# Kernel tuning notes

Hardware: AMD Instinct MI355X
Metric: run time of the kernel (lower is better)

Reference implementation:

```python
import jax, jax.numpy as jnp
import numpy as np

B, S, D = 4, 1024, 768
V, L, K = 50265, 256, 4
COMMIT = 0.25
PERP_W = 0.1


def _l2n(a):
    return a * jax.lax.rsqrt(jnp.sum(a * a, axis=-1, keepdims=True) + 1e-12)


def setup_inputs() -> dict:
    key = jax.random.key(0)
    ks = jax.random.split(key, 4)
    return {
        'x': jax.random.normal(ks[0], (B, S, D), dtype=jnp.float32),
        'codebook': jax.random.normal(ks[1], (V, D), dtype=jnp.float32) * 0.02,
        'W_in': jax.random.normal(ks[2], (D, L), dtype=jnp.float32) / np.sqrt(D),
        'b_in': jnp.zeros((L,), dtype=jnp.float32),
        'W_code': jax.random.normal(ks[3], (D, L), dtype=jnp.float32) / np.sqrt(D),
        'b_code': jnp.zeros((L,), dtype=jnp.float32),
    }


def reference(x, codebook, W_in, b_in, W_code, b_code):
    # project inputs and codebook to latent space, L2-normalize
    zi = _l2n(x.reshape(-1, D) @ W_in + b_in)                 # [N, L]
    # original normalizes latent codebook twice (idempotent) then stop-grads
    zc = jax.lax.stop_gradient(_l2n(codebook @ W_code + b_code))  # [V, L]
    # squared euclidean distance: |a|^2 + |b|^2 - 2 a.b
    d = (jnp.sum(zi * zi, -1, keepdims=True)
         + jnp.sum(zc * zc, -1)[None, :]
         - 2.0 * (zi @ zc.T)).reshape(B, S, V)                # [B, S, V]
    # top-k nearest codes (exact top_k as reference for approx_min_k)
    idx = jax.lax.top_k(-d, K)[1]                             # [B, S, K] int32
    # quantize: gather codes and average over k (top_k_avg path)
    quantized = jnp.take(codebook, idx, axis=0).mean(axis=-2) # [B, S, D]
    # codebook stats without materializing [B,S,K,V] one-hot
    counts = jnp.zeros((V,), x.dtype).at[idx.reshape(-1)].add(1.0)
    codebook_usage = jnp.sum(counts > 0).astype(x.dtype) / V / K
    avg_probs = counts / (B * S * K)
    log_perp = -jnp.sum(avg_probs * jnp.log(avg_probs + 1e-10))
    perplexity = jnp.exp(log_perp)
    # train losses (quantized is stop-gradient'd before loss in original)
    q_sg = jax.lax.stop_gradient(quantized)

    def train_loss(q, t):
        e = jnp.mean((jax.lax.stop_gradient(q) - t) ** 2) * COMMIT
        ql = jnp.mean((q - jax.lax.stop_gradient(t)) ** 2)
        return e + ql

    loss = train_loss(q_sg, x)
    loss = loss + train_loss(q_sg @ W_code + b_code, x @ W_in + b_in)
    loss = loss + PERP_W * log_perp
    # straight-through estimator
    out = x + jax.lax.stop_gradient(q_sg - x)
    return out, loss, perplexity, codebook_usage
```

## Files before the change

kernel.cpp:

```cpp
#include <hip/hip_runtime.h>
#include <math.h>

#define N_TOK 4096
#define DDIM  768
#define LDIM  256
#define VNUM  50265
#define VPAD  50304
#define NCTILE 393
#define NGRP  8
#define KSEL  4
#define M3    3145728

#define WS_ZI_PRE 0
#define WS_ZI     (WS_ZI_PRE + N_TOK*LDIM)
#define WS_ZC     (WS_ZI + N_TOK*LDIM)
#define WS_ZCB    (WS_ZC + VPAD*LDIM)
#define WS_QUANT  WS_ZCB
#define WS_CAND   (WS_ZCB + VPAD*LDIM/2)
#define WS_IDX    (WS_CAND + N_TOK*64)
#define WS_COUNTS (WS_IDX + N_TOK*4)
#define WS_ACCUM  (WS_COUNTS + VPAD)

typedef __attribute__((ext_vector_type(8))) short short8;
typedef __attribute__((ext_vector_type(4))) float f32x4;

__device__ __forceinline__ unsigned short f2bf(float f) {
    unsigned u = __float_as_uint(f);
    u += 0x7fffu + ((u >> 16) & 1u);
    return (unsigned short)(u >> 16);
}

__device__ __forceinline__ bool better(float v1, int i1, float v2, int i2) {
    return (v1 > v2) || (v1 == v2 && i1 < i2);
}

template<int K>
__device__ __forceinline__ void insertK(float (&v)[K], int (&ix)[K], float nv, int ni) {
    if (!better(nv, ni, v[K-1], ix[K-1])) return;
    v[K-1] = nv; ix[K-1] = ni;
    #pragma unroll
    for (int j = K-1; j > 0; j--) {
        if (better(v[j], ix[j], v[j-1], ix[j-1])) {
            float tv = v[j]; v[j] = v[j-1]; v[j-1] = tv;
            int ti = ix[j]; ix[j] = ix[j-1]; ix[j-1] = ti;
        } else break;
    }
}

__global__ __launch_bounds__(256) void gemm_k(
    const float* __restrict__ A, const float* __restrict__ W,
    const float* __restrict__ bias, float* __restrict__ out_pre,
    float* __restrict__ out_norm, unsigned short* __restrict__ out_bf,
    const float* __restrict__ target, float* __restrict__ accum_slot,
    int M, int mode)
{
    __shared__ float a_s[32*64];
    __shared__ float w_s[32*256];
    const int tid = threadIdx.x;
    const int tx = tid & 31, ty = tid >> 5;
    const int mbase = blockIdx.x * 64;

    float acc[8][8];
    #pragma unroll
    for (int i = 0; i < 8; i++)
        #pragma unroll
        for (int j = 0; j < 8; j++) acc[i][j] = 0.f;

    for (int kk = 0; kk < DDIM; kk += 32) {
        __syncthreads();
        #pragma unroll
        for (int s = 0; s < 2; s++) {
            int slot = tid + s*256;
            int row = slot >> 3, kc = (slot & 7) << 2;
            int gr = mbase + row; if (gr >= M) gr = M - 1;
            float4 v = *(const float4*)&A[(size_t)gr*DDIM + kk + kc];
            a_s[(kc+0)*64 + row] = v.x;
            a_s[(kc+1)*64 + row] = v.y;
            a_s[(kc+2)*64 + row] = v.z;
            a_s[(kc+3)*64 + row] = v.w;
        }
        #pragma unroll
        for (int s = 0; s < 8; s++) {
            int slot = tid + s*256;
            int r = slot >> 6, c = (slot & 63) << 2;
            *(float4*)&w_s[r*256 + c] = *(const float4*)&W[(size_t)(kk + r)*LDIM + c];
        }
        __syncthreads();
        #pragma unroll
        for (int k = 0; k < 32; k++) {
            float4 a0 = *(float4*)&a_s[k*64 + ty*8];
            float4 a1 = *(float4*)&a_s[k*64 + ty*8 + 4];
            float4 w0 = *(float4*)&w_s[k*256 + tx*4];
            float4 w1 = *(float4*)&w_s[k*256 + 128 + tx*4];
            float am[8] = {a0.x,a0.y,a0.z,a0.w,a1.x,a1.y,a1.z,a1.w};
            float wn[8] = {w0.x,w0.y,w0.z,w0.w,w1.x,w1.y,w1.z,w1.w};
            #pragma unroll
            for (int i = 0; i < 8; i++)
                #pragma unroll
                for (int j = 0; j < 8; j++)
                    acc[i][j] = fmaf(am[i], wn[j], acc[i][j]);
        }
    }

    float bn[8];
    #pragma unroll
    for (int j = 0; j < 8; j++) {
        int col = (j < 4) ? (tx*4 + j) : (128 + tx*4 + (j-4));
        bn[j] = bias[col];
    }
    #pragma unroll
    for (int i = 0; i < 8; i++)
        #pragma unroll
        for (int j = 0; j < 8; j++) acc[i][j] += bn[j];

    if (mode == 1) {
        #pragma unroll
        for (int i = 0; i < 8; i++) {
            int gr = mbase + ty*8 + i;
            if (gr < M) {
                *(float4*)&out_pre[(size_t)gr*LDIM + tx*4] =
                    make_float4(acc[i][0], acc[i][1], acc[i][2], acc[i][3]);
                *(float4*)&out_pre[(size_t)gr*LDIM + 128 + tx*4] =
                    make_float4(acc[i][4], acc[i][5], acc[i][6], acc[i][7]);
            }
        }
    }
    if (mode == 1 || mode == 2) {
        #pragma unroll
        for (int i = 0; i < 8; i++) {
            float s = 0.f;
            #pragma unroll
            for (int j = 0; j < 8; j++) s += acc[i][j]*acc[i][j];
            #pragma unroll
            for (int m = 16; m >= 1; m >>= 1) s += __shfl_xor(s, m, 64);
            float sc = 1.0f / sqrtf(s + 1e-12f);
            int gr = mbase + ty*8 + i;
            bool wr = (mode == 2) || (gr < M);
            if (wr) {
                float p[8];
                #pragma unroll
                for (int j = 0; j < 8; j++) p[j] = acc[i][j]*sc;
                *(float4*)&out_norm[(size_t)gr*LDIM + tx*4] = make_float4(p[0],p[1],p[2],p[3]);
                *(float4*)&out_norm[(size_t)gr*LDIM + 128 + tx*4] = make_float4(p[4],p[5],p[6],p[7]);
                if (out_bf) {
                    ushort4 b0, b1;
                    b0.x = f2bf(p[0]); b0.y = f2bf(p[1]); b0.z = f2bf(p[2]); b0.w = f2bf(p[3]);
                    b1.x = f2bf(p[4]); b1.y = f2bf(p[5]); b1.z = f2bf(p[6]); b1.w = f2bf(p[7]);
                    *(ushort4*)&out_bf[(size_t)gr*LDIM + tx*4] = b0;
                    *(ushort4*)&out_bf[(size_t)gr*LDIM + 128 + tx*4] = b1;
                }
            }
        }
    }
    if (mode == 3) {
        float ls = 0.f;
        #pragma unroll
        for (int i = 0; i < 8; i++) {
            int gr = mbase + ty*8 + i;
            if (gr < M) {
                #pragma unroll
                for (int j = 0; j < 8; j++) {
                    int col = (j < 4) ? (tx*4 + j) : (128 + tx*4 + (j-4));
                    float dd = acc[i][j] - target[(size_t)gr*LDIM + col];
                    ls = fmaf(dd, dd, ls);
                }
            }
        }
        #pragma unroll
        for (int off = 32; off >= 1; off >>= 1) ls += __shfl_down(ls, off, 64);
        __syncthreads();
        if ((tid & 63) == 0) a_s[tid >> 6] = ls;
        __syncthreads();
        if (tid == 0) atomicAdd(accum_slot, a_s[0]+a_s[1]+a_s[2]+a_s[3]);
    }
}

__device__ __forceinline__ void stage_chunk(
    const unsigned short* __restrict__ zcb, unsigned char* smem,
    int ci, int wave, int lane, int g)
{
    const int ct = g + (ci >> 2) * NGRP;
    const int chunk = ci & 3;
    unsigned char* lbase = smem + (ci & 1) * 16384 + wave * 4096;
    const size_t rowbase = (size_t)ct * 128 + wave * 32;
    #pragma unroll
    for (int j = 0; j < 4; j++) {
        const unsigned short* gp = zcb + (rowbase + j*8 + (lane >> 3)) * LDIM
                                       + chunk*64 + (lane & 7)*8;
        __builtin_amdgcn_global_load_lds(
            (const __attribute__((address_space(1))) void*)gp,
            (__attribute__((address_space(3))) void*)(lbase + j*1024), 16, 0, 0);
    }
}

__global__ __launch_bounds__(256, 2) void filter_kernel(
    const float* __restrict__ zi, const unsigned short* __restrict__ zcb,
    int* __restrict__ cand)
{
    __shared__ unsigned char smem[49152];
    float* mv = (float*)smem;
    int*   mi = (int*)(smem + 24576);

    const int tid = threadIdx.x;
    const int wave = tid >> 6, lane = tid & 63;
    const int wq = wave >> 1, wc = wave & 1;
    const int l15 = lane & 15, l4 = lane >> 4;
    const int qbase = blockIdx.x * 64 + wq * 32;
    const int g = blockIdx.y;

    short8 afrag[2][8];
    #pragma unroll
    for (int qi = 0; qi < 2; qi++)
        #pragma unroll
        for (int ks = 0; ks < 8; ks++) {
            const float* src = zi + (size_t)(qbase + qi*16 + l15)*LDIM + ks*32 + l4*8;
            float4 v0 = *(const float4*)src;
            float4 v1 = *(const float4*)(src + 4);
            short8 a;
            a[0] = (short)f2bf(v0.x); a[1] = (short)f2bf(v0.y);
            a[2] = (short)f2bf(v0.z); a[3] = (short)f2bf(v0.w);
            a[4] = (short)f2bf(v1.x); a[5] = (short)f2bf(v1.y);
            a[6] = (short)f2bf(v1.z); a[7] = (short)f2bf(v1.w);
            afrag[qi][ks] = a;
        }

    float tv[2][4][3]; int tix[2][4][3];
    #pragma unroll
    for (int qi = 0; qi < 2; qi++)
        #pragma unroll
        for (int rr = 0; rr < 4; rr++)
            #pragma unroll
            for (int j = 0; j < 3; j++) { tv[qi][rr][j] = -1e30f; tix[qi][rr][j] = 0x7fffffff; }

    f32x4 acc[2][4];
    #pragma unroll
    for (int qi = 0; qi < 2; qi++)
        #pragma unroll
        for (int tc = 0; tc < 4; tc++) acc[qi][tc] = (f32x4)(0.f);

    const int nct = (g == 0) ? 50 : 49;
    const int NCk = nct * 4;

    stage_chunk(zcb, smem, 0, wave, lane, g);

    for (int ci = 0; ci < NCk; ci++) {
        __syncthreads();
        if (ci + 1 < NCk) stage_chunk(zcb, smem, ci + 1, wave, lane, g);

        const unsigned short* lb = (const unsigned short*)(smem + (ci & 1)*16384);
        #pragma unroll
        for (int ks2 = 0; ks2 < 2; ks2++) {
            const int kf = (ci & 3)*2 + ks2;
            #pragma unroll
            for (int tc = 0; tc < 4; tc++) {
                const short8 b = *(const short8*)&lb[(wc*64 + tc*16 + l15)*64 + ks2*32 + l4*8];
                acc[0][tc] = __builtin_amdgcn_mfma_f32_16x16x32_bf16(afrag[0][kf], b, acc[0][tc], 0, 0, 0);
                acc[1][tc] = __builtin_amdgcn_mfma_f32_16x16x32_bf16(afrag[1][kf], b, acc[1][tc], 0, 0, 0);
            }
        }

        if ((ci & 3) == 3) {
            const int cb0 = (g + (ci >> 2)*NGRP)*128 + wc*64 + l15;
            #pragma unroll
            for (int tc = 0; tc < 4; tc++) {
                const int col = cb0 + tc*16;
                const bool ok = col < VNUM;
                #pragma unroll
                for (int qi = 0; qi < 2; qi++) {
                    #pragma unroll
                    for (int rr = 0; rr < 4; rr++) {
                        float v = acc[qi][tc][rr];
                        if (ok) insertK<3>(tv[qi][rr], tix[qi][rr], v, col);
                    }
                    acc[qi][tc] = (f32x4)(0.f);
                }
            }
        }
    }

    __syncthreads();
    #pragma unroll
    for (int qi = 0; qi < 2; qi++)
        #pragma unroll
        for (int rr = 0; rr < 4; rr++) {
            const int qb = wq*32 + qi*16 + l4*4 + rr;
            const int slot = (wc*16 + l15)*3;
            #pragma unroll
            for (int j = 0; j < 3; j++) {
                mv[qb*96 + slot + j] = tv[qi][rr][j];
                mi[qb*96 + slot + j] = tix[qi][rr][j];
            }
        }
    __syncthreads();
    if (tid < 64) {
        float v[8]; int ix[8];
        #pragma unroll
        for (int j = 0; j < 8; j++) { v[j] = -1e30f; ix[j] = 0x7fffffff; }
        for (int s = 0; s < 96; s++) insertK<8>(v, ix, mv[tid*96 + s], mi[tid*96 + s]);
        const int q = blockIdx.x*64 + tid;
        #pragma unroll
        for (int j = 0; j < 8; j++) cand[(size_t)q*64 + g*8 + j] = ix[j];
    }
}

__global__ __launch_bounds__(256) void rescore_kernel(
    const float* __restrict__ zi, const float* __restrict__ zc,
    const int* __restrict__ cand, int* __restrict__ idx4)
{
    __shared__ float zi_s[256];
    __shared__ float sval[64];
    __shared__ int   sidx[64];
    const int q = blockIdx.x;
    const int t = threadIdx.x;
    if (t < 64) *(float4*)&zi_s[t*4] = *(const float4*)&zi[(size_t)q*LDIM + t*4];
    __syncthreads();

    const int j = t >> 2, l4 = t & 3;
    int idx = cand[(size_t)q*64 + j];
    const bool valid = (unsigned)idx < (unsigned)VNUM;
    const float* r = zc + (size_t)(valid ? idx : 0)*LDIM;
    float dot = 0.f, nsq = 0.f;
    #pragma unroll
    for (int i = 0; i < 16; i++) {
        float4 v = *(const float4*)&r[i*16 + l4*4];
        float4 z = *(const float4*)&zi_s[i*16 + l4*4];
        dot = fmaf(v.x, z.x, fmaf(v.y, z.y, fmaf(v.z, z.z, fmaf(v.w, z.w, dot))));
        nsq = fmaf(v.x, v.x, fmaf(v.y, v.y, fmaf(v.z, v.z, fmaf(v.w, v.w, nsq))));
    }
    dot += __shfl_xor(dot, 1, 64); dot += __shfl_xor(dot, 2, 64);
    nsq += __shfl_xor(nsq, 1, 64); nsq += __shfl_xor(nsq, 2, 64);
    const float sc = valid ? (dot - 0.5f*nsq) : -1e30f;
    if (l4 == 0) { sval[j] = sc; sidx[j] = valid ? idx : 0x7fffffff; }
    __syncthreads();

    if (t < 64) {
        float v[4] = {-1e30f, -1e30f, -1e30f, -1e30f};
        int ix[4] = {0x7fffffff, 0x7fffffff, 0x7fffffff, 0x7fffffff};
        insertK<4>(v, ix, sval[t], sidx[t]);
        #pragma unroll
        for (int m = 1; m < 64; m <<= 1) {
            float ov[4]; int oi[4];
            #pragma unroll
            for (int s = 0; s < 4; s++) {
                ov[s] = __shfl_xor(v[s], m, 64);
                oi[s] = __shfl_xor(ix[s], m, 64);
            }
            #pragma unroll
            for (int s = 0; s < 4; s++) insertK<4>(v, ix, ov[s], oi[s]);
        }
        if (t == 0) {
            #pragma unroll
            for (int s = 0; s < 4; s++) idx4[q*4 + s] = ix[s];
        }
    }
}

__global__ __launch_bounds__(192) void gather_kernel(
    const float* __restrict__ x, const float* __restrict__ cb,
    const int* __restrict__ idx4, float* __restrict__ quant,
    float* __restrict__ out, float* __restrict__ counts,
    float* __restrict__ accum)
{
    __shared__ float red[3];
    const int n = blockIdx.x;
    const int t = threadIdx.x;
    const int i0 = idx4[n*4+0], i1 = idx4[n*4+1], i2 = idx4[n*4+2], i3 = idx4[n*4+3];
    if (t < 4) atomicAdd(&counts[idx4[n*4+t]], 1.0f);
    const int d = t*4;
    float4 c0 = *(const float4*)&cb[(size_t)i0*DDIM + d];
    float4 c1 = *(const float4*)&cb[(size_t)i1*DDIM + d];
    float4 c2 = *(const float4*)&cb[(size_t)i2*DDIM + d];
    float4 c3 = *(const float4*)&cb[(size_t)i3*DDIM + d];
    float4 xv = *(const float4*)&x[(size_t)n*DDIM + d];
    float4 qv;
    qv.x = (((c0.x + c1.x) + c2.x) + c3.x) * 0.25f;
    qv.y = (((c0.y + c1.y) + c2.y) + c3.y) * 0.25f;
    qv.z = (((c0.z + c1.z) + c2.z) + c3.z) * 0.25f;
    qv.w = (((c0.w + c1.w) + c2.w) + c3.w) * 0.25f;
    float4 o;
    o.x = xv.x + (qv.x - xv.x);
    o.y = xv.y + (qv.y - xv.y);
    o.z = xv.z + (qv.z - xv.z);
    o.w = xv.w + (qv.w - xv.w);
    *(float4*)&quant[(size_t)n*DDIM + d] = qv;
    *(float4*)&out[(size_t)n*DDIM + d] = o;
    float d0 = qv.x - xv.x, d1 = qv.y - xv.y, d2 = qv.z - xv.z, d3 = qv.w - xv.w;
    float ls = d0*d0 + d1*d1 + d2*d2 + d3*d3;
    #pragma unroll
    for (int off = 32; off >= 1; off >>= 1) ls += __shfl_down(ls, off, 64);
    if ((t & 63) == 0) red[t >> 6] = ls;
    __syncthreads();
    if (t == 0) atomicAdd(accum, red[0] + red[1] + red[2]);
}

__global__ __launch_bounds__(256) void stats_kernel(
    const float* __restrict__ counts, float* __restrict__ accum)
{
    __shared__ float redE[4], redN[4];
    int v = blockIdx.x*256 + threadIdx.x;
    float ent = 0.f, nnz = 0.f;
    if (v < VNUM) {
        float c = counts[v];
        if (c > 0.f) {
            float p = c * (1.0f/16384.0f);
            ent = p * logf(p + 1e-10f);
            nnz = 1.f;
        }
    }
    #pragma unroll
    for (int off = 32; off >= 1; off >>= 1) {
        ent += __shfl_down(ent, off, 64);
        nnz += __shfl_down(nnz, off, 64);
    }
    int t = threadIdx.x;
    if ((t & 63) == 0) { redE[t>>6] = ent; redN[t>>6] = nnz; }
    __syncthreads();
    if (t == 0) {
        atomicAdd(accum+2, redE[0]+redE[1]+redE[2]+redE[3]);
        atomicAdd(accum+3, redN[0]+redN[1]+redN[2]+redN[3]);
    }
}

__global__ void final_kernel(const float* __restrict__ accum, float* __restrict__ out)
{
    float logp = -accum[2];
    float m1 = accum[0] * (1.0f / (float)M3);
    float m2 = accum[1] * (1.0f / (float)(N_TOK*LDIM));
    float loss = (m1*0.25f + m1) + (m2*0.25f + m2) + 0.1f*logp;
    out[M3+0] = loss;
    out[M3+1] = expf(logp);
    out[M3+2] = (accum[3] / (float)VNUM) / (float)KSEL;
}

extern "C" void kernel_launch(void* const* d_in, const int* in_sizes, int n_in,
                              void* d_out, int out_size, void* d_ws, size_t ws_size,
                              hipStream_t stream)
{
    const float* x      = (const float*)d_in[0];
    const float* cb     = (const float*)d_in[1];
    const float* W_in   = (const float*)d_in[2];
    const float* b_in   = (const float*)d_in[3];
    const float* W_code = (const float*)d_in[4];
    const float* b_code = (const float*)d_in[5];
    float* out = (float*)d_out;
    float* w   = (float*)d_ws;

    float* zi_pre = w + WS_ZI_PRE;
    float* zi     = w + WS_ZI;
    float* zc     = w + WS_ZC;
    unsigned short* zcb = (unsigned short*)(w + WS_ZCB);
    float* quant  = w + WS_QUANT;
    int*   cand   = (int*)(w + WS_CAND);
    int*   idx4   = (int*)(w + WS_IDX);
    float* counts = w + WS_COUNTS;
    float* accum  = w + WS_ACCUM;

    hipMemsetAsync(counts, 0, (VPAD + 8)*sizeof(float), stream);

    gemm_k<<<N_TOK/64, 256, 0, stream>>>(x, W_in, b_in, zi_pre, zi, nullptr,
                                         nullptr, nullptr, N_TOK, 1);
    gemm_k<<<VPAD/64, 256, 0, stream>>>(cb, W_code, b_code, nullptr, zc, zcb,
                                        nullptr, nullptr, VNUM, 2);
    filter_kernel<<<dim3(N_TOK/64, NGRP), 256, 0, stream>>>(zi, zcb, cand);
    rescore_kernel<<<N_TOK, 256, 0, stream>>>(zi, zc, cand, idx4);
    gather_kernel<<<N_TOK, 192, 0, stream>>>(x, cb, idx4, quant, out, counts, accum);
    stats_kernel<<<(VNUM + 255)/256, 256, 0, stream>>>(counts, accum);
    gemm_k<<<N_TOK/64, 256, 0, stream>>>(quant, W_code, b_code, nullptr, nullptr, nullptr,
                                         zi_pre, accum+1, N_TOK, 3);
    final_kernel<<<1, 1, 0, stream>>>(accum, out);
}
```

Measured before the change: 1.237 ms.

## Restructure filter kernel: larger query blocks, 4-stage swizzled LDS pipeline, shuffle merge

```diff
diff --git a/kernel.cpp b/kernel.cpp
--- a/kernel.cpp
+++ b/kernel.cpp
@@ -6,8 +6,9 @@
 #define LDIM  256
 #define VNUM  50265
 #define VPAD  50304
-#define NCTILE 393
-#define NGRP  8
+#define NT64  786
+#define NGRP  16
+#define QBLK  256
 #define KSEL  4
 #define M3    3145728
 
@@ -175,45 +176,39 @@
     }
 }
 
+
 __device__ __forceinline__ void stage_chunk(
     const unsigned short* __restrict__ zcb, unsigned char* smem,
     int ci, int wave, int lane, int g)
 {
-    const int ct = g + (ci >> 2) * NGRP;
-    const int chunk = ci & 3;
-    unsigned char* lbase = smem + (ci & 1) * 16384 + wave * 4096;
-    const size_t rowbase = (size_t)ct * 128 + wave * 32;
-    #pragma unroll
-    for (int j = 0; j < 4; j++) {
-        const unsigned short* gp = zcb + (rowbase + j*8 + (lane >> 3)) * LDIM
-                                       + chunk*64 + (lane & 7)*8;
-        __builtin_amdgcn_global_load_lds(
-            (const __attribute__((address_space(1))) void*)gp,
-            (__attribute__((address_space(3))) void*)(lbase + j*1024), 16, 0, 0);
-    }
-}
-
-__global__ __launch_bounds__(256, 2) void filter_kernel(
+    const int T  = g + (ci >> 2) * NGRP;
+    const int kc = ci & 3;
+    const int r_local = wave*8 + (lane >> 3);
+    const int sg = (lane & 7) ^ (lane >> 3);
+    const unsigned short* gp = zcb + (size_t)(T*64 + r_local)*LDIM + kc*64 + sg*8;
+    unsigned char* lp = smem + (ci & 3)*8192 + wave*1024 + lane*16;
+    __builtin_amdgcn_global_load_lds(
+        (const __attribute__((address_space(1))) void*)gp,
+        (__attribute__((address_space(3))) void*)lp, 16, 0, 0);
+}
+
+__global__ __launch_bounds__(512, 2) void filter_kernel(
     const float* __restrict__ zi, const unsigned short* __restrict__ zcb,
     int* __restrict__ cand)
 {
-    __shared__ unsigned char smem[49152];
-    float* mv = (float*)smem;
-    int*   mi = (int*)(smem + 24576);
-
+    __shared__ unsigned char smem[32768];
     const int tid = threadIdx.x;
     const int wave = tid >> 6, lane = tid & 63;
-    const int wq = wave >> 1, wc = wave & 1;
     const int l15 = lane & 15, l4 = lane >> 4;
-    const int qbase = blockIdx.x * 64 + wq * 32;
+    const int qbase = blockIdx.x * QBLK + wave * 32;
     const int g = blockIdx.y;
 
     short8 afrag[2][8];
     #pragma unroll
-    for (int qi = 0; qi < 2; qi++)
+    for (int qt = 0; qt < 2; qt++)
         #pragma unroll
         for (int ks = 0; ks < 8; ks++) {
-            const float* src = zi + (size_t)(qbase + qi*16 + l15)*LDIM + ks*32 + l4*8;
+            const float* src = zi + (size_t)(qbase + qt*16 + l15)*LDIM + ks*32 + l4*8;
             float4 v0 = *(const float4*)src;
             float4 v1 = *(const float4*)(src + 4);
             short8 a;
@@ -221,86 +216,94 @@
             a[2] = (short)f2bf(v0.z); a[3] = (short)f2bf(v0.w);
             a[4] = (short)f2bf(v1.x); a[5] = (short)f2bf(v1.y);
             a[6] = (short)f2bf(v1.z); a[7] = (short)f2bf(v1.w);
-            afrag[qi][ks] = a;
+            afrag[qt][ks] = a;
         }
 
     float tv[2][4][3]; int tix[2][4][3];
     #pragma unroll
-    for (int qi = 0; qi < 2; qi++)
+    for (int qt = 0; qt < 2; qt++)
         #pragma unroll
         for (int rr = 0; rr < 4; rr++)
             #pragma unroll
-            for (int j = 0; j < 3; j++) { tv[qi][rr][j] = -1e30f; tix[qi][rr][j] = 0x7fffffff; }
+            for (int j = 0; j < 3; j++) { tv[qt][rr][j] = -1e30f; tix[qt][rr][j] = 0x7fffffff; }
 
     f32x4 acc[2][4];
     #pragma unroll
-    for (int qi = 0; qi < 2; qi++)
-        #pragma unroll
-        for (int tc = 0; tc < 4; tc++) acc[qi][tc] = (f32x4)(0.f);
-
-    const int nct = (g == 0) ? 50 : 49;
+    for (int qt = 0; qt < 2; qt++)
+        #pragma unroll
+        for (int tc = 0; tc < 4; tc++) acc[qt][tc] = (f32x4)(0.f);
+
+    const int nct = (g < 2) ? 50 : 49;
     const int NCk = nct * 4;
 
     stage_chunk(zcb, smem, 0, wave, lane, g);
+    stage_chunk(zcb, smem, 1, wave, lane, g);
+    stage_chunk(zcb, smem, 2, wave, lane, g);
 
     for (int ci = 0; ci < NCk; ci++) {
-        __syncthreads();
-        if (ci + 1 < NCk) stage_chunk(zcb, smem, ci + 1, wave, lane, g);
-
-        const unsigned short* lb = (const unsigned short*)(smem + (ci & 1)*16384);
+        __builtin_amdgcn_s_waitcnt(0x0F72);
+        __builtin_amdgcn_s_barrier();
+        asm volatile("" ::: "memory");
+        int nx = ci + 3; if (nx >= NCk) nx -= NCk;
+        stage_chunk(zcb, smem, nx, wave, lane, g);
+
+        const unsigned short* lb = (const unsigned short*)(smem + (ci & 3)*8192);
+        const int kc = ci & 3;
         #pragma unroll
         for (int ks2 = 0; ks2 < 2; ks2++) {
-            const int kf = (ci & 3)*2 + ks2;
+            const int kf = kc*2 + ks2;
             #pragma unroll
             for (int tc = 0; tc < 4; tc++) {
-                const short8 b = *(const short8*)&lb[(wc*64 + tc*16 + l15)*64 + ks2*32 + l4*8];
+                const int c = tc*16 + l15;
+                const int slot = (ks2*4 + l4) ^ (c & 7);
+                const short8 b = *(const short8*)&lb[c*64 + slot*8];
                 acc[0][tc] = __builtin_amdgcn_mfma_f32_16x16x32_bf16(afrag[0][kf], b, acc[0][tc], 0, 0, 0);
                 acc[1][tc] = __builtin_amdgcn_mfma_f32_16x16x32_bf16(afrag[1][kf], b, acc[1][tc], 0, 0, 0);
             }
         }
 
         if ((ci & 3) == 3) {
-            const int cb0 = (g + (ci >> 2)*NGRP)*128 + wc*64 + l15;
+            const int T = g + (ci >> 2)*NGRP;
             #pragma unroll
             for (int tc = 0; tc < 4; tc++) {
-                const int col = cb0 + tc*16;
+                const int col = T*64 + tc*16 + l15;
                 const bool ok = col < VNUM;
                 #pragma unroll
-                for (int qi = 0; qi < 2; qi++) {
+                for (int qt = 0; qt < 2; qt++) {
                     #pragma unroll
                     for (int rr = 0; rr < 4; rr++) {
-                        float v = acc[qi][tc][rr];
-                        if (ok) insertK<3>(tv[qi][rr], tix[qi][rr], v, col);
+                        float v = acc[qt][tc][rr];
+                        if (ok) insertK<3>(tv[qt][rr], tix[qt][rr], v, col);
                     }
-                    acc[qi][tc] = (f32x4)(0.f);
+                    acc[qt][tc] = (f32x4)(0.f);
                 }
             }
         }
     }
 
-    __syncthreads();
-    #pragma unroll
-    for (int qi = 0; qi < 2; qi++)
+    #pragma unroll
+    for (int qt = 0; qt < 2; qt++)
         #pragma unroll
         for (int rr = 0; rr < 4; rr++) {
-            const int qb = wq*32 + qi*16 + l4*4 + rr;
-            const int slot = (wc*16 + l15)*3;
-            #pragma unroll
-            for (int j = 0; j < 3; j++) {
-                mv[qb*96 + slot + j] = tv[qi][rr][j];
-                mi[qb*96 + slot + j] = tix[qi][rr][j];
-            }
-        }
-    __syncthreads();
-    if (tid < 64) {
-        float v[8]; int ix[8];
-        #pragma unroll
-        for (int j = 0; j < 8; j++) { v[j] = -1e30f; ix[j] = 0x7fffffff; }
-        for (int s = 0; s < 96; s++) insertK<8>(v, ix, mv[tid*96 + s], mi[tid*96 + s]);
-        const int q = blockIdx.x*64 + tid;
-        #pragma unroll
-        for (int j = 0; j < 8; j++) cand[(size_t)q*64 + g*8 + j] = ix[j];
-    }
+            float mv[4] = { tv[qt][rr][0], tv[qt][rr][1], tv[qt][rr][2], -1e30f };
+            int   mi[4] = { tix[qt][rr][0], tix[qt][rr][1], tix[qt][rr][2], 0x7fffffff };
+            #pragma unroll
+            for (int m = 1; m < 16; m <<= 1) {
+                float ov[4]; int oi[4];
+                #pragma unroll
+                for (int s = 0; s < 4; s++) {
+                    ov[s] = __shfl_xor(mv[s], m, 64);
+                    oi[s] = __shfl_xor(mi[s], m, 64);
+                }
+                #pragma unroll
+                for (int s = 0; s < 4; s++) insertK<4>(mv, mi, ov[s], oi[s]);
+            }
+            if (l15 == 0) {
+                const int q = qbase + qt*16 + l4*4 + rr;
+                #pragma unroll
+                for (int j = 0; j < 4; j++) cand[(size_t)q*64 + g*4 + j] = mi[j];
+            }
+        }
 }
 
 __global__ __launch_bounds__(256) void rescore_kernel(
@@ -461,7 +464,7 @@
                                          nullptr, nullptr, N_TOK, 1);
     gemm_k<<<VPAD/64, 256, 0, stream>>>(cb, W_code, b_code, nullptr, zc, zcb,
                                         nullptr, nullptr, VNUM, 2);
-    filter_kernel<<<dim3(N_TOK/64, NGRP), 256, 0, stream>>>(zi, zcb, cand);
+    filter_kernel<<<dim3(N_TOK/QBLK, NGRP), 512, 0, stream>>>(zi, zcb, cand);
     rescore_kernel<<<N_TOK, 256, 0, stream>>>(zi, zc, cand, idx4);
     gather_kernel<<<N_TOK, 192, 0, stream>>>(x, cb, idx4, quant, out, counts, accum);
     stats_kernel<<<(VNUM + 255)/256, 256, 0, stream>>>(counts, accum);
```

Result: slower. 1.269 ms (+2.6%).
